# Performance work log

Hardware: AMD Instinct MI355X
Metric: run time of the kernel (lower is better)

The kernel has to match this reference:

```python
import jax, jax.numpy as jnp
import numpy as np

B, N, C, H = 2, 2048, 1024, 16
ATTN_BIAS = -7.625   # ~ -log(N), sigmoid-attention bias
ATTN_TEMP = 0.0      # attn scaled by exp(attn_temp)


def setup_inputs() -> dict:
    key = jax.random.key(0)
    k1, k2, k3 = jax.random.split(key, 3)
    x = jax.random.normal(k1, (B, N, C), jnp.float32)
    # nn.Linear weights: y = x @ W.T (bias=False)
    w_qkv = jax.random.normal(k2, (3 * C, C), jnp.float32) * (C ** -0.5)
    w_proj = jax.random.normal(k3, (C, C), jnp.float32) * (C ** -0.5)
    return {"x": x, "w_qkv": w_qkv, "w_proj": w_proj}


def reference(x, w_qkv, w_proj):
    b, n, c = x.shape
    dh = c // H
    scale = dh ** -0.5
    # qkv projection -> (3, B, H, N, Dh)
    qkv = (x @ w_qkv.T).reshape(b, n, 3, H, dh).transpose(2, 0, 3, 1, 4)
    q, k, v = qkv[0], qkv[1], qkv[2]
    attn = jnp.einsum('bhnd,bhmd->bhnm', q * scale, k)  # [B,H,N,N]
    attn = attn * jnp.exp(jnp.float32(ATTN_TEMP)) + jnp.float32(ATTN_BIAS)
    attn_matrix = jax.nn.sigmoid(attn)  # attn_activ_fn = sigmoid
    attn_times_v = jnp.einsum('bhnm,bhmd->bhnd', attn_matrix, v)
    attn_times_v = attn_times_v.transpose(0, 2, 1, 3).reshape(b, n, c)
    attn_proj = attn_times_v @ w_proj.T
    return attn_matrix, attn_times_v, attn_proj
```

## Files before the change

### kernel.cpp

```cpp
#include <hip/hip_runtime.h>


typedef short short8 __attribute__((ext_vector_type(8)));
typedef unsigned short ushort8v __attribute__((ext_vector_type(8)));
typedef float f32x4 __attribute__((ext_vector_type(4)));

#define DEV static __device__ __forceinline__

DEV unsigned short f2bf(float f) {
  unsigned u = __builtin_bit_cast(unsigned, f);
  u += 0x7FFFu + ((u >> 16) & 1u);
  return (unsigned short)(u >> 16);
}

DEV float sigmoid_fast(float z) {
  float e = __builtin_amdgcn_exp2f(z * -1.44269504f);
  return __builtin_amdgcn_rcpf(1.0f + e);
}

__global__ void cvt_f32_bf16(const float* __restrict__ in,
                             unsigned short* __restrict__ out, int n4) {
  int i = blockIdx.x * blockDim.x + threadIdx.x;
  if (i >= n4) return;
  float4 f = ((const float4*)in)[i];
  ushort4 o;
  o.x = f2bf(f.x); o.y = f2bf(f.y); o.z = f2bf(f.z); o.w = f2bf(f.w);
  ((ushort4*)out)[i] = o;
}

template<int MODE>
__global__ __launch_bounds__(256) void gemm_bf16_nt(
    const unsigned short* __restrict__ A, const unsigned short* __restrict__ B,
    unsigned short* __restrict__ outQKV, float* __restrict__ outF,
    int M, int N, int K) {
  __shared__ __align__(16) unsigned short At[128 * 72];
  __shared__ __align__(16) unsigned short Bt[128 * 72];
  const int t = threadIdx.x;
  const int row0 = blockIdx.x * 128, col0 = blockIdx.y * 128;
  const int w = t >> 6, lane = t & 63, lm = lane & 15, quad = lane >> 4;
  const int mb = (w >> 1) * 64, nb = (w & 1) * 64;

  f32x4 acc[4][4];
#pragma unroll
  for (int i = 0; i < 4; i++)
#pragma unroll
    for (int j = 0; j < 4; j++) acc[i][j] = (f32x4)0.0f;

  for (int k0 = 0; k0 < K; k0 += 64) {
#pragma unroll
    for (int i = 0; i < 4; i++) {
      int c = t + 256 * i;
      int r = c >> 3, cc = c & 7;
      *(int4*)&At[r * 72 + cc * 8] =
          *(const int4*)&A[(size_t)(row0 + r) * K + k0 + cc * 8];
      *(int4*)&Bt[r * 72 + cc * 8] =
          *(const int4*)&B[(size_t)(col0 + r) * K + k0 + cc * 8];
    }
    __syncthreads();
#pragma unroll
    for (int kk = 0; kk < 64; kk += 32) {
      short8 af[4], bf[4];
#pragma unroll
      for (int i = 0; i < 4; i++)
        af[i] = *(const short8*)&At[(mb + 16 * i + lm) * 72 + kk + quad * 8];
#pragma unroll
      for (int j = 0; j < 4; j++)
        bf[j] = *(const short8*)&Bt[(nb + 16 * j + lm) * 72 + kk + quad * 8];
#pragma unroll
      for (int i = 0; i < 4; i++)
#pragma unroll
        for (int j = 0; j < 4; j++)
          acc[i][j] = __builtin_amdgcn_mfma_f32_16x16x32_bf16(
              af[i], bf[j], acc[i][j], 0, 0, 0);
    }
    __syncthreads();
  }

#pragma unroll
  for (int i = 0; i < 4; i++) {
#pragma unroll
    for (int j = 0; j < 4; j++) {
#pragma unroll
      for (int r = 0; r < 4; r++) {
        int rM = row0 + mb + 16 * i + quad * 4 + r;
        int cN = col0 + nb + 16 * j + lm;
        float v = acc[i][j][r];
        if (MODE == 0) {
          int s = cN >> 10, hh = (cN >> 6) & 15, d = cN & 63;
          int b = rM >> 11, nl = rM & 2047;
          outQKV[(size_t)s * 4194304 +
                 ((size_t)((b << 4) + hh) * 2048 + nl) * 64 + d] = f2bf(v);
        } else {
          outF[(size_t)rM * N + cN] = v;
        }
      }
    }
  }
}

__global__ __launch_bounds__(256) void attn_sigmoid(
    const unsigned short* __restrict__ Q, const unsigned short* __restrict__ Kk,
    const unsigned short* __restrict__ V, float* __restrict__ Pout,
    float* __restrict__ atvF, unsigned short* __restrict__ atvB) {
  __shared__ __align__(16) unsigned short Kt[128 * 72];
  __shared__ __align__(16) unsigned short Vt[64 * 136];
  __shared__ __align__(16) unsigned short Pl[128 * 136];

  const int t = threadIdx.x;
  const int qt = blockIdx.x & 15, bh = blockIdx.x >> 4;
  const int b = bh >> 4, h = bh & 15;
  const int q0 = qt * 128;
  const int w = t >> 6, lane = t & 63, lm = lane & 15, quad = lane >> 4;

  const unsigned short* qh = Q + (size_t)bh * 2048 * 64;
  const unsigned short* kh = Kk + (size_t)bh * 2048 * 64;
  const unsigned short* vh = V + (size_t)bh * 2048 * 64;
  float* pbase = Pout + (size_t)bh * 2048 * 2048;

  short8 qf[2][2];
#pragma unroll
  for (int i = 0; i < 2; i++)
#pragma unroll
    for (int kc = 0; kc < 2; kc++)
      qf[i][kc] = *(const short8*)&qh[(size_t)(q0 + w * 32 + 16 * i + lm) * 64 +
                                      kc * 32 + quad * 8];

  f32x4 oacc[2][4];
#pragma unroll
  for (int i = 0; i < 2; i++)
#pragma unroll
    for (int n = 0; n < 4; n++) oacc[i][n] = (f32x4)0.0f;

  for (int kt = 0; kt < 16; kt++) {
    const int k0 = kt * 128;
#pragma unroll
    for (int i = 0; i < 4; i++) {
      int c = t + 256 * i;
      int r = c >> 3, cc = c & 7;
      *(int4*)&Kt[r * 72 + cc * 8] =
          *(const int4*)&kh[(size_t)(k0 + r) * 64 + cc * 8];
    }
    {
      int r = t & 127;
      int cb = t >> 7;
#pragma unroll
      for (int i = 0; i < 4; i++) {
        int cc = cb + 2 * i;
        ushort8v vv = *(const ushort8v*)&vh[(size_t)(k0 + r) * 64 + cc * 8];
#pragma unroll
        for (int l = 0; l < 8; l++) Vt[(cc * 8 + l) * 136 + r] = vv[l];
      }
    }
    __syncthreads();

    f32x4 sacc[2][8];
#pragma unroll
    for (int i = 0; i < 2; i++)
#pragma unroll
      for (int j = 0; j < 8; j++) sacc[i][j] = (f32x4)0.0f;
#pragma unroll
    for (int kc = 0; kc < 2; kc++) {
      short8 bk[8];
#pragma unroll
      for (int j = 0; j < 8; j++)
        bk[j] = *(const short8*)&Kt[(16 * j + lm) * 72 + kc * 32 + quad * 8];
#pragma unroll
      for (int i = 0; i < 2; i++)
#pragma unroll
        for (int j = 0; j < 8; j++)
          sacc[i][j] = __builtin_amdgcn_mfma_f32_16x16x32_bf16(
              qf[i][kc], bk[j], sacc[i][j], 0, 0, 0);
    }

#pragma unroll
    for (int i = 0; i < 2; i++) {
#pragma unroll
      for (int j = 0; j < 8; j++) {
#pragma unroll
        for (int r = 0; r < 4; r++) {
          float s = sigmoid_fast(sacc[i][j][r] * 0.125f - 7.625f);
          int rt = w * 32 + 16 * i + quad * 4 + r;
          int ct = 16 * j + lm;
          __builtin_nontemporal_store(
              s, &pbase[(size_t)(q0 + rt) * 2048 + k0 + ct]);
          Pl[rt * 136 + ct] = f2bf(s);
        }
      }
    }
    __syncthreads();

#pragma unroll
    for (int kc = 0; kc < 4; kc++) {
      short8 ap[2], bv[4];
#pragma unroll
      for (int i = 0; i < 2; i++)
        ap[i] = *(const short8*)&Pl[(w * 32 + 16 * i + lm) * 136 + kc * 32 +
                                    quad * 8];
#pragma unroll
      for (int n = 0; n < 4; n++)
        bv[n] = *(const short8*)&Vt[(16 * n + lm) * 136 + kc * 32 + quad * 8];
#pragma unroll
      for (int i = 0; i < 2; i++)
#pragma unroll
        for (int n = 0; n < 4; n++)
          oacc[i][n] = __builtin_amdgcn_mfma_f32_16x16x32_bf16(
              ap[i], bv[n], oacc[i][n], 0, 0, 0);
    }
    __syncthreads();
  }

#pragma unroll
  for (int i = 0; i < 2; i++) {
#pragma unroll
    for (int n = 0; n < 4; n++) {
#pragma unroll
      for (int r = 0; r < 4; r++) {
        int grow = q0 + w * 32 + 16 * i + quad * 4 + r;
        int gcol = h * 64 + 16 * n + lm;
        size_t idx = ((size_t)(b * 2048 + grow)) * 1024 + gcol;
        float v = oacc[i][n][r];
        atvF[idx] = v;
        atvB[idx] = f2bf(v);
      }
    }
  }
}

extern "C" void kernel_launch(void* const* d_in, const int* in_sizes, int n_in,
                              void* d_out, int out_size, void* d_ws,
                              size_t ws_size, hipStream_t stream) {
  const float* x = (const float*)d_in[0];
  const float* w_qkv = (const float*)d_in[1];
  const float* w_proj = (const float*)d_in[2];

  float* Pout = (float*)d_out;
  float* atvOut = (float*)d_out + 134217728;
  float* projOut = (float*)d_out + 138412032;

  unsigned char* ws = (unsigned char*)d_ws;
  unsigned short* xbf = (unsigned short*)(ws + 0);
  unsigned short* wqkvbf = (unsigned short*)(ws + 8388608);
  unsigned short* wprojbf = (unsigned short*)(ws + 14680064);
  unsigned short* qb = (unsigned short*)(ws + 16777216);
  unsigned short* kb = (unsigned short*)(ws + 25165824);
  unsigned short* vb = (unsigned short*)(ws + 33554432);
  unsigned short* atvbf = (unsigned short*)(ws + 41943040);

  cvt_f32_bf16<<<4096, 256, 0, stream>>>(x, xbf, 1048576);
  cvt_f32_bf16<<<3072, 256, 0, stream>>>(w_qkv, wqkvbf, 786432);
  cvt_f32_bf16<<<1024, 256, 0, stream>>>(w_proj, wprojbf, 262144);

  gemm_bf16_nt<0><<<dim3(32, 24), 256, 0, stream>>>(xbf, wqkvbf, qb, nullptr,
                                                    4096, 3072, 1024);

  attn_sigmoid<<<512, 256, 0, stream>>>(qb, kb, vb, Pout, atvOut, atvbf);

  gemm_bf16_nt<1><<<dim3(32, 8), 256, 0, stream>>>(atvbf, wprojbf, nullptr,
                                                   projOut, 4096, 1024, 1024);
}
```

Measured before the change: 762.0 us.

## Use direct global-to-LDS loads with XOR swizzle and vectorized transposed P stores

```diff
diff --git a/kernel.cpp b/kernel.cpp
--- a/kernel.cpp
+++ b/kernel.cpp
@@ -13,8 +13,20 @@
   return (unsigned short)(u >> 16);
 }
 
-DEV float sigmoid_fast(float z) {
-  float e = __builtin_amdgcn_exp2f(z * -1.44269504f);
+DEV unsigned cvt_pk_bf16(float lo, float hi) {
+  unsigned r;
+  asm("v_cvt_pk_bf16_f32 %0, %1, %2" : "=v"(r) : "v"(lo), "v"(hi));
+  return r;
+}
+
+DEV void gload_lds16(const void* g, void* l) {
+  __builtin_amdgcn_global_load_lds(
+      (const __attribute__((address_space(1))) unsigned*)g,
+      (__attribute__((address_space(3))) unsigned*)l, 16, 0, 0);
+}
+
+DEV float sigmoid_from_s(float s) {
+  float e = __builtin_amdgcn_exp2f(__builtin_fmaf(s, -0.18033688f, 11.00054968f));
   return __builtin_amdgcn_rcpf(1.0f + e);
 }
 
@@ -33,12 +45,14 @@
     const unsigned short* __restrict__ A, const unsigned short* __restrict__ B,
     unsigned short* __restrict__ outQKV, float* __restrict__ outF,
     int M, int N, int K) {
-  __shared__ __align__(16) unsigned short At[128 * 72];
-  __shared__ __align__(16) unsigned short Bt[128 * 72];
+  __shared__ __align__(16) unsigned short At[128 * 64];
+  __shared__ __align__(16) unsigned short Bt[128 * 64];
   const int t = threadIdx.x;
   const int row0 = blockIdx.x * 128, col0 = blockIdx.y * 128;
   const int w = t >> 6, lane = t & 63, lm = lane & 15, quad = lane >> 4;
   const int mb = (w >> 1) * 64, nb = (w & 1) * 64;
+  const int sr = w * 32 + (lane >> 3);
+  const int l8 = lane & 7;
 
   f32x4 acc[4][4];
 #pragma unroll
@@ -48,24 +62,26 @@
 
   for (int k0 = 0; k0 < K; k0 += 64) {
 #pragma unroll
-    for (int i = 0; i < 4; i++) {
-      int c = t + 256 * i;
-      int r = c >> 3, cc = c & 7;
-      *(int4*)&At[r * 72 + cc * 8] =
-          *(const int4*)&A[(size_t)(row0 + r) * K + k0 + cc * 8];
-      *(int4*)&Bt[r * 72 + cc * 8] =
-          *(const int4*)&B[(size_t)(col0 + r) * K + k0 + cc * 8];
-    }
-    __syncthreads();
-#pragma unroll
-    for (int kk = 0; kk < 64; kk += 32) {
+    for (int ii = 0; ii < 4; ii++) {
+      int rg = sr + 8 * ii;
+      int cc = l8 ^ (rg & 7);
+      gload_lds16(&A[(size_t)(row0 + rg) * K + k0 + cc * 8],
+                  &At[(w * 32 + 8 * ii) * 64]);
+      gload_lds16(&B[(size_t)(col0 + rg) * K + k0 + cc * 8],
+                  &Bt[(w * 32 + 8 * ii) * 64]);
+    }
+    __syncthreads();
+#pragma unroll
+    for (int kc = 0; kc < 2; kc++) {
       short8 af[4], bf[4];
 #pragma unroll
       for (int i = 0; i < 4; i++)
-        af[i] = *(const short8*)&At[(mb + 16 * i + lm) * 72 + kk + quad * 8];
+        af[i] = *(const short8*)&At[(mb + 16 * i + lm) * 64 +
+                                    (((kc << 2) + quad) ^ (lm & 7)) * 8];
 #pragma unroll
       for (int j = 0; j < 4; j++)
-        bf[j] = *(const short8*)&Bt[(nb + 16 * j + lm) * 72 + kk + quad * 8];
+        bf[j] = *(const short8*)&Bt[(nb + 16 * j + lm) * 64 +
+                                    (((kc << 2) + quad) ^ (lm & 7)) * 8];
 #pragma unroll
       for (int i = 0; i < 4; i++)
 #pragma unroll
@@ -102,15 +118,17 @@
     const unsigned short* __restrict__ Q, const unsigned short* __restrict__ Kk,
     const unsigned short* __restrict__ V, float* __restrict__ Pout,
     float* __restrict__ atvF, unsigned short* __restrict__ atvB) {
-  __shared__ __align__(16) unsigned short Kt[128 * 72];
+  __shared__ __align__(16) unsigned short Kt[128 * 64];
   __shared__ __align__(16) unsigned short Vt[64 * 136];
   __shared__ __align__(16) unsigned short Pl[128 * 136];
 
   const int t = threadIdx.x;
-  const int qt = blockIdx.x & 15, bh = blockIdx.x >> 4;
+  const int swz = (blockIdx.x & 7) * 64 + (blockIdx.x >> 3);
+  const int qt = swz & 15, bh = swz >> 4;
   const int b = bh >> 4, h = bh & 15;
   const int q0 = qt * 128;
   const int w = t >> 6, lane = t & 63, lm = lane & 15, quad = lane >> 4;
+  const int sr = w * 32 + (lane >> 3), l8 = lane & 7;
 
   const unsigned short* qh = Q + (size_t)bh * 2048 * 64;
   const unsigned short* kh = Kk + (size_t)bh * 2048 * 64;
@@ -134,21 +152,20 @@
   for (int kt = 0; kt < 16; kt++) {
     const int k0 = kt * 128;
 #pragma unroll
-    for (int i = 0; i < 4; i++) {
-      int c = t + 256 * i;
-      int r = c >> 3, cc = c & 7;
-      *(int4*)&Kt[r * 72 + cc * 8] =
-          *(const int4*)&kh[(size_t)(k0 + r) * 64 + cc * 8];
+    for (int ii = 0; ii < 4; ii++) {
+      int rg = sr + 8 * ii;
+      int cc = l8 ^ (rg & 7);
+      gload_lds16(&kh[(size_t)(k0 + rg) * 64 + cc * 8],
+                  &Kt[(w * 32 + 8 * ii) * 64]);
     }
     {
-      int r = t & 127;
-      int cb = t >> 7;
+      int r = t & 127, cb = t >> 7;
 #pragma unroll
       for (int i = 0; i < 4; i++) {
-        int cc = cb + 2 * i;
-        ushort8v vv = *(const ushort8v*)&vh[(size_t)(k0 + r) * 64 + cc * 8];
-#pragma unroll
-        for (int l = 0; l < 8; l++) Vt[(cc * 8 + l) * 136 + r] = vv[l];
+        int cc2 = cb + 2 * i;
+        ushort8v vv = *(const ushort8v*)&vh[(size_t)(k0 + r) * 64 + cc2 * 8];
+#pragma unroll
+        for (int l = 0; l < 8; l++) Vt[(cc2 * 8 + l) * 136 + r] = vv[l];
       }
     }
     __syncthreads();
@@ -163,31 +180,32 @@
       short8 bk[8];
 #pragma unroll
       for (int j = 0; j < 8; j++)
-        bk[j] = *(const short8*)&Kt[(16 * j + lm) * 72 + kc * 32 + quad * 8];
+        bk[j] = *(const short8*)&Kt[(16 * j + lm) * 64 +
+                                    (((kc << 2) + quad) ^ (lm & 7)) * 8];
 #pragma unroll
       for (int i = 0; i < 2; i++)
 #pragma unroll
         for (int j = 0; j < 8; j++)
           sacc[i][j] = __builtin_amdgcn_mfma_f32_16x16x32_bf16(
-              qf[i][kc], bk[j], sacc[i][j], 0, 0, 0);
+              bk[j], qf[i][kc], sacc[i][j], 0, 0, 0);
     }
 
 #pragma unroll
     for (int i = 0; i < 2; i++) {
 #pragma unroll
       for (int j = 0; j < 8; j++) {
-#pragma unroll
-        for (int r = 0; r < 4; r++) {
-          float s = sigmoid_fast(sacc[i][j][r] * 0.125f - 7.625f);
-          int rt = w * 32 + 16 * i + quad * 4 + r;
-          int ct = 16 * j + lm;
-          __builtin_nontemporal_store(
-              s, &pbase[(size_t)(q0 + rt) * 2048 + k0 + ct]);
-          Pl[rt * 136 + ct] = f2bf(s);
-        }
-      }
-    }
-    __syncthreads();
+        f32x4 p;
+#pragma unroll
+        for (int r = 0; r < 4; r++) p[r] = sigmoid_from_s(sacc[i][j][r]);
+        __builtin_nontemporal_store(
+            p, (f32x4*)&pbase[(size_t)(q0 + w * 32 + 16 * i + lm) * 2048 +
+                              k0 + 16 * j + quad * 4]);
+        uint2 pw;
+        pw.x = cvt_pk_bf16(p[0], p[1]);
+        pw.y = cvt_pk_bf16(p[2], p[3]);
+        *(uint2*)&Pl[(w * 32 + 16 * i + lm) * 136 + 16 * j + quad * 4] = pw;
+      }
+    }
 
 #pragma unroll
     for (int kc = 0; kc < 4; kc++) {
```

Result: faster. 724.0 us (-5.0%).
